# Performance work log

Measured on AMD Instinct MI355X. Metric: run time of the kernel, lower is better.

Reference implementation:

```python
import jax, jax.numpy as jnp
import numpy as np

N_EMBD = 1024
N_HEAD = 16
HEAD_SIZE = N_EMBD // N_HEAD  # 64
HEAD_INDEX = 0
# ALiBi slope: x = (2**8)**(1/n_head); slope = 1 / x**(head_index+1)
SLOPE = 1.0 / ((2.0 ** 8) ** (1.0 / N_HEAD)) ** (HEAD_INDEX + 1)
B, T = 4, 4096


def setup_inputs() -> dict:
    key = jax.random.key(0)
    kx, kq, kk, kv = jax.random.split(key, 4)
    x = jax.random.normal(kx, (B, T, N_EMBD), dtype=jnp.float32)
    wq = jax.random.normal(kq, (HEAD_SIZE, N_EMBD), dtype=jnp.float32) * 0.02
    wk = jax.random.normal(kk, (HEAD_SIZE, N_EMBD), dtype=jnp.float32) * 0.02
    wv = jax.random.normal(kv, (HEAD_SIZE, N_EMBD), dtype=jnp.float32) * 0.02
    return {"x": x, "wq": wq, "wk": wk, "wv": wv}


def reference(x, wq, wk, wv):
    Bq, Tq, C = x.shape
    q = jnp.einsum('btc,hc->bth', x, wq)  # [B,T,Hd]
    k = jnp.einsum('btc,hc->bth', x, wk)
    v = jnp.einsum('btc,hc->bth', x, wv)
    # NOTE: original scales by C**-0.5 where C = n_embd (full dim), not head_size
    wei = jnp.einsum('bth,bsh->bts', q, k) * (C ** -0.5)  # [B,T,T]
    idx = jnp.arange(Tq)
    distance = idx[None, :] - idx[:, None]  # [T,T], j - i
    wei = wei + distance.astype(wei.dtype) * jnp.asarray(SLOPE, wei.dtype)
    causal = distance <= 0  # tril: key index j <= query index i
    wei = jnp.where(causal[None, :, :], wei, -jnp.inf)
    wei = jax.nn.softmax(wei, axis=-1)
    out = jnp.einsum('bts,bsh->bth', wei, v)  # [B,T,Hd]
    return out
```

## Files before the change

### kernel.cpp

```cpp
#include <hip/hip_runtime.h>
#include <hip/hip_bf16.h>
#include <stdint.h>
#include <math.h>

typedef __attribute__((ext_vector_type(8))) short bf16x8;
typedef __attribute__((ext_vector_type(4))) float f32x4;

#define TSEQ 4096
#define LOG2E 1.44269504088896340736f
#define SLOPE 0.70710678118654752440f
#define SL2E (SLOPE * LOG2E)

__device__ __forceinline__ unsigned short f32_to_bf16(float f) {
  union { float f; unsigned int u; } v; v.f = f;
  unsigned int r = v.u + 0x7fffu + ((v.u >> 16) & 1u);
  return (unsigned short)(r >> 16);
}

__device__ __forceinline__ unsigned int pk2(float a, float b) {
  union { __hip_bfloat162 h; unsigned int u; } c;
  c.h = __float22bfloat162_rn(make_float2(a, b));
  return c.u;
}
__device__ __forceinline__ bf16x8 cvt8(f32x4 a, f32x4 b) {
  union { unsigned int u[4]; bf16x8 v; } r;
  r.u[0] = pk2(a[0], a[1]); r.u[1] = pk2(a[2], a[3]);
  r.u[2] = pk2(b[0], b[1]); r.u[3] = pk2(b[2], b[3]);
  return r.v;
}

__device__ __forceinline__ void async_cp16(const void* g, void* l) {
  __builtin_amdgcn_global_load_lds(
      (const __attribute__((address_space(1))) unsigned int*)g,
      (__attribute__((address_space(3))) unsigned int*)l, 16, 0, 0);
}

__global__ __launch_bounds__(256) void init_kernel(
    const float* __restrict__ wq, const float* __restrict__ wk,
    const float* __restrict__ wv, unsigned short* __restrict__ Wb,
    unsigned short* __restrict__ vt) {
  int tid = blockIdx.x * 256 + threadIdx.x;
  if (tid < 24576) {
    int lane = tid & 63, s = (tid >> 6) & 31, nt = (tid >> 11) & 3, t = tid >> 13;
    int n = nt * 16 + (lane & 15);
    int k = s * 32 + (lane >> 4) * 8;
    const float* src = (t == 0 ? wq : (t == 1 ? wk : wv)) + (size_t)n * 1024 + k;
    f32x4 a = *(const f32x4*)src;
    f32x4 b = *(const f32x4*)(src + 4);
    if (t == 0) {
#pragma unroll
      for (int j = 0; j < 4; ++j) { a[j] *= 0.03125f; b[j] *= 0.03125f; }
    }
    *(bf16x8*)(Wb + (size_t)tid * 8) = cvt8(a, b);
  }
  int b2 = tid >> 15, off = (tid & 32767) * 2;
  *(unsigned int*)(vt + (size_t)b2 * 327680 + 262144 + off) = 0x3F803F80u;
}

__global__ __launch_bounds__(256, 2) void proj_kernel(
    const float* __restrict__ x, const unsigned short* __restrict__ Wb,
    unsigned short* __restrict__ qb, unsigned short* __restrict__ kb,
    unsigned short* __restrict__ vt) {
  __shared__ float xbuf[2][64][64];
  __shared__ unsigned short wbuf[2][12][2][64][8];

  const int lane = threadIdx.x & 63;
  const int wave = threadIdx.x >> 6;
  const int l16 = lane & 15, quad = lane >> 4;
  const int R0 = blockIdx.x * 64;

  f32x4 acc[12];
#pragma unroll
  for (int i = 0; i < 12; ++i) acc[i] = (f32x4){0.f, 0.f, 0.f, 0.f};

  const float* xsrc[4];
#pragma unroll
  for (int i = 0; i < 4; ++i) {
    int row = wave * 16 + i * 4 + quad;
    int g = l16 ^ (row & 15);
    xsrc[i] = x + (size_t)(R0 + row) * 1024 + g * 4;
  }
  const unsigned short* wsrc[6];
#pragma unroll
  for (int j = 0; j < 6; ++j) {
    int q = wave * 6 + j;
    wsrc[j] = Wb + ((size_t)((q >> 1) * 32 + (q & 1)) * 64 + lane) * 8;
  }

#pragma unroll
  for (int i = 0; i < 4; ++i)
    async_cp16(xsrc[i], &xbuf[0][wave * 16 + i * 4][0]);
#pragma unroll
  for (int j = 0; j < 6; ++j) {
    int q = wave * 6 + j;
    async_cp16(wsrc[j], &wbuf[0][q >> 1][q & 1][0][0]);
  }
  __syncthreads();

#pragma unroll 1
  for (int step = 0; step < 16; ++step) {
    const int cur = step & 1;
    if (step + 1 < 16) {
      const int nxt = 1 - cur;
#pragma unroll
      for (int i = 0; i < 4; ++i)
        async_cp16(xsrc[i] + (step + 1) * 64, &xbuf[nxt][wave * 16 + i * 4][0]);
#pragma unroll
      for (int j = 0; j < 6; ++j) {
        int q = wave * 6 + j;
        async_cp16(wsrc[j] + (size_t)(step + 1) * 2 * 64 * 8,
                   &wbuf[nxt][q >> 1][q & 1][0][0]);
      }
    }
#pragma unroll
    for (int ss = 0; ss < 2; ++ss) {
      const float* base = &xbuf[cur][wave * 16 + l16][0];
      f32x4 a0 = *(const f32x4*)(base + ((ss * 8 + quad * 2) ^ l16) * 4);
      f32x4 a1 = *(const f32x4*)(base + ((ss * 8 + quad * 2 + 1) ^ l16) * 4);
      bf16x8 af = cvt8(a0, a1);
#pragma unroll
      for (int ci = 0; ci < 12; ++ci) {
        bf16x8 wfr = *(const bf16x8*)&wbuf[cur][ci][ss][lane][0];
        acc[ci] = __builtin_amdgcn_mfma_f32_16x16x32_bf16(af, wfr, acc[ci], 0, 0, 0);
      }
    }
    __syncthreads();
  }

#pragma unroll
  for (int ci = 0; ci < 12; ++ci) {
#pragma unroll
    for (int r = 0; r < 4; ++r) {
      int row = R0 + wave * 16 + quad * 4 + r;
      unsigned short hv = f32_to_bf16(acc[ci][r]);
      if (ci < 4) {
        qb[(size_t)row * 64 + ci * 16 + l16] = hv;
      } else if (ci < 8) {
        kb[(size_t)row * 64 + (ci - 4) * 16 + l16] = hv;
      } else {
        int b = row >> 12, tt = row & 4095;
        vt[((size_t)b * 80 + (ci - 8) * 16 + l16) * TSEQ + tt] = hv;
      }
    }
  }
}

__global__ __launch_bounds__(256, 4) void attn_kernel(
    const unsigned short* __restrict__ qb, const unsigned short* __restrict__ kb,
    const unsigned short* __restrict__ vt, float* __restrict__ out) {
  __shared__ unsigned short pbuf[4][16][40];
  __shared__ float obuf[4][5][16][17];

  const int lane = threadIdx.x & 63;
  const int wave = threadIdx.x >> 6;
  const int l16 = lane & 15, quad = lane >> 4;
  const int tid = blockIdx.x;
  const int b = tid & 3;
  const int r0 = (tid >> 2) << 4;
  const int j0 = (r0 > 112) ? (r0 - 112) : 0;
  const int jb = j0 + wave * 32;

  const unsigned short* kbase = kb + (size_t)b * TSEQ * 64;
  const unsigned short* vbase = vt + (size_t)b * 80 * TSEQ;

  const unsigned short* qrow = qb + (size_t)(b * TSEQ + r0 + l16) * 64 + quad * 8;
  bf16x8 qa0 = *(const bf16x8*)qrow;
  bf16x8 qa1 = *(const bf16x8*)(qrow + 32);

  f32x4 o[5];
#pragma unroll
  for (int dt = 0; dt < 5; ++dt) o[dt] = (f32x4){0.f, 0.f, 0.f, 0.f};

  const int irel = jb + l16 - r0 - quad * 4;
  const float fb = SL2E * (float)irel;

#pragma unroll
  for (int nt = 0; nt < 2; ++nt) {
    const unsigned short* krow = kbase + (size_t)(jb + nt * 16 + l16) * 64 + quad * 8;
    f32x4 sa = (f32x4){0.f, 0.f, 0.f, 0.f};
    sa = __builtin_amdgcn_mfma_f32_16x16x32_bf16(qa0, *(const bf16x8*)krow, sa, 0, 0, 0);
    sa = __builtin_amdgcn_mfma_f32_16x16x32_bf16(qa1, *(const bf16x8*)(krow + 32), sa, 0, 0, 0);
#pragma unroll
    for (int r = 0; r < 4; ++r) {
      float arg = fmaf(sa[r], LOG2E, fb + SL2E * (float)(nt * 16 - r));
      float p = exp2f(arg);
      if (irel + nt * 16 - r > 0) p = 0.f;
      pbuf[wave][quad * 4 + r][nt * 16 + l16] = f32_to_bf16(p);
    }
  }
  bf16x8 pa = *(const bf16x8*)&pbuf[wave][l16][quad * 8];

#pragma unroll
  for (int dt = 0; dt < 5; ++dt) {
    const unsigned short* vrow = vbase + (size_t)(dt * 16 + l16) * TSEQ + jb + quad * 8;
    o[dt] = __builtin_amdgcn_mfma_f32_16x16x32_bf16(pa, *(const bf16x8*)vrow, o[dt], 0, 0, 0);
  }

#pragma unroll
  for (int dt = 0; dt < 5; ++dt)
#pragma unroll
    for (int r = 0; r < 4; ++r)
      obuf[wave][dt][quad * 4 + r][l16] = o[dt][r];

  __syncthreads();

  const int rr = threadIdx.x >> 4;
  const int c0 = (threadIdx.x & 15) * 4;
  const int dt = c0 >> 4, cc = c0 & 15;
  float l = obuf[0][4][rr][0] + obuf[1][4][rr][0] + obuf[2][4][rr][0] + obuf[3][4][rr][0];
  float invl = 1.0f / l;
  f32x4 res;
#pragma unroll
  for (int i = 0; i < 4; ++i)
    res[i] = (obuf[0][dt][rr][cc + i] + obuf[1][dt][rr][cc + i] +
              obuf[2][dt][rr][cc + i] + obuf[3][dt][rr][cc + i]) * invl;
  *(f32x4*)(out + (size_t)(b * TSEQ + r0 + rr) * 64 + c0) = res;
}

extern "C" void kernel_launch(void* const* d_in, const int* in_sizes, int n_in,
                              void* d_out, int out_size, void* d_ws, size_t ws_size,
                              hipStream_t stream) {
  const float* x  = (const float*)d_in[0];
  const float* wq = (const float*)d_in[1];
  const float* wk = (const float*)d_in[2];
  const float* wv = (const float*)d_in[3];
  float* out = (float*)d_out;

  char* ws = (char*)d_ws;
  unsigned short* Wb = (unsigned short*)(ws);
  unsigned short* qb = (unsigned short*)(ws + 393216);
  unsigned short* kb = (unsigned short*)(ws + 393216 + 2097152);
  unsigned short* vt = (unsigned short*)(ws + 393216 + 2 * 2097152);

  init_kernel<<<512, 256, 0, stream>>>(wq, wk, wv, Wb, vt);
  proj_kernel<<<256, 256, 0, stream>>>(x, Wb, qb, kb, vt);
  attn_kernel<<<1024, 256, 0, stream>>>(qb, kb, vt, out);
}
```

Baseline: 125.3 us.

## Triple-buffer projection loads with explicit vmcnt waits; synthesize ones row in registers

The projection kernel moves from double to triple buffering. Loads are issued two steps ahead, and the full __syncthreads is replaced by manual s_waitcnt vmcnt counts plus raw s_barrier, so global loads can stay in flight across iterations. The ones row in vt, used to compute the softmax denominator, is no longer written by init_kernel. The attention kernel instead builds it as a register constant, which shrinks the init launch and cuts the vt stride from 80 to 64 rows. The larger LDS footprint may lower occupancy, and the hand-counted vmcnt values must exactly match the number of outstanding loads.

```diff
diff --git a/kernel.cpp b/kernel.cpp
--- a/kernel.cpp
+++ b/kernel.cpp
@@ -37,32 +37,28 @@
 
 __global__ __launch_bounds__(256) void init_kernel(
     const float* __restrict__ wq, const float* __restrict__ wk,
-    const float* __restrict__ wv, unsigned short* __restrict__ Wb,
-    unsigned short* __restrict__ vt) {
+    const float* __restrict__ wv, unsigned short* __restrict__ Wb) {
   int tid = blockIdx.x * 256 + threadIdx.x;
-  if (tid < 24576) {
-    int lane = tid & 63, s = (tid >> 6) & 31, nt = (tid >> 11) & 3, t = tid >> 13;
-    int n = nt * 16 + (lane & 15);
-    int k = s * 32 + (lane >> 4) * 8;
-    const float* src = (t == 0 ? wq : (t == 1 ? wk : wv)) + (size_t)n * 1024 + k;
-    f32x4 a = *(const f32x4*)src;
-    f32x4 b = *(const f32x4*)(src + 4);
-    if (t == 0) {
-#pragma unroll
-      for (int j = 0; j < 4; ++j) { a[j] *= 0.03125f; b[j] *= 0.03125f; }
-    }
-    *(bf16x8*)(Wb + (size_t)tid * 8) = cvt8(a, b);
-  }
-  int b2 = tid >> 15, off = (tid & 32767) * 2;
-  *(unsigned int*)(vt + (size_t)b2 * 327680 + 262144 + off) = 0x3F803F80u;
-}
-
-__global__ __launch_bounds__(256, 2) void proj_kernel(
+  if (tid >= 24576) return;
+  int lane = tid & 63, s = (tid >> 6) & 31, nt = (tid >> 11) & 3, t = tid >> 13;
+  int n = nt * 16 + (lane & 15);
+  int k = s * 32 + (lane >> 4) * 8;
+  const float* src = (t == 0 ? wq : (t == 1 ? wk : wv)) + (size_t)n * 1024 + k;
+  f32x4 a = *(const f32x4*)src;
+  f32x4 b = *(const f32x4*)(src + 4);
+  if (t == 0) {
+#pragma unroll
+    for (int j = 0; j < 4; ++j) { a[j] *= 0.03125f; b[j] *= 0.03125f; }
+  }
+  *(bf16x8*)(Wb + (size_t)tid * 8) = cvt8(a, b);
+}
+
+__global__ __launch_bounds__(256) void proj_kernel(
     const float* __restrict__ x, const unsigned short* __restrict__ Wb,
     unsigned short* __restrict__ qb, unsigned short* __restrict__ kb,
     unsigned short* __restrict__ vt) {
-  __shared__ float xbuf[2][64][64];
-  __shared__ unsigned short wbuf[2][12][2][64][8];
+  __shared__ float xbuf[3][64][64];
+  __shared__ unsigned short wbuf[3][12][2][64][8];
 
   const int lane = threadIdx.x & 63;
   const int wave = threadIdx.x >> 6;
@@ -87,31 +83,31 @@
     wsrc[j] = Wb + ((size_t)((q >> 1) * 32 + (q & 1)) * 64 + lane) * 8;
   }
 
-#pragma unroll
-  for (int i = 0; i < 4; ++i)
-    async_cp16(xsrc[i], &xbuf[0][wave * 16 + i * 4][0]);
-#pragma unroll
-  for (int j = 0; j < 6; ++j) {
-    int q = wave * 6 + j;
-    async_cp16(wsrc[j], &wbuf[0][q >> 1][q & 1][0][0]);
-  }
-  __syncthreads();
+  auto stage = [&](int s, int bi) {
+#pragma unroll
+    for (int i = 0; i < 4; ++i)
+      async_cp16(xsrc[i] + s * 64, &xbuf[bi][wave * 16 + i * 4][0]);
+#pragma unroll
+    for (int j = 0; j < 6; ++j) {
+      int q = wave * 6 + j;
+      async_cp16(wsrc[j] + (size_t)s * 1024, &wbuf[bi][q >> 1][q & 1][0][0]);
+    }
+  };
+
+  stage(0, 0);
+  stage(1, 1);
 
 #pragma unroll 1
   for (int step = 0; step < 16; ++step) {
-    const int cur = step & 1;
-    if (step + 1 < 16) {
-      const int nxt = 1 - cur;
-#pragma unroll
-      for (int i = 0; i < 4; ++i)
-        async_cp16(xsrc[i] + (step + 1) * 64, &xbuf[nxt][wave * 16 + i * 4][0]);
-#pragma unroll
-      for (int j = 0; j < 6; ++j) {
-        int q = wave * 6 + j;
-        async_cp16(wsrc[j] + (size_t)(step + 1) * 2 * 64 * 8,
-                   &wbuf[nxt][q >> 1][q & 1][0][0]);
-      }
-    }
+    const int cur = step % 3;
+    if (step + 2 < 16) stage(step + 2, (step + 2) % 3);
+    __builtin_amdgcn_sched_barrier(0);
+    if (step < 14)       asm volatile("s_waitcnt vmcnt(20)" ::: "memory");
+    else if (step == 14) asm volatile("s_waitcnt vmcnt(10)" ::: "memory");
+    else                 asm volatile("s_waitcnt vmcnt(0)" ::: "memory");
+    __builtin_amdgcn_sched_barrier(0);
+    __builtin_amdgcn_s_barrier();
+    __builtin_amdgcn_sched_barrier(0);
 #pragma unroll
     for (int ss = 0; ss < 2; ++ss) {
       const float* base = &xbuf[cur][wave * 16 + l16][0];
@@ -124,7 +120,8 @@
         acc[ci] = __builtin_amdgcn_mfma_f32_16x16x32_bf16(af, wfr, acc[ci], 0, 0, 0);
       }
     }
-    __syncthreads();
+    __builtin_amdgcn_sched_barrier(0);
+    __builtin_amdgcn_s_barrier();
   }
 
 #pragma unroll
@@ -139,7 +136,7 @@
         kb[(size_t)row * 64 + (ci - 4) * 16 + l16] = hv;
       } else {
         int b = row >> 12, tt = row & 4095;
-        vt[((size_t)b * 80 + (ci - 8) * 16 + l16) * TSEQ + tt] = hv;
+        vt[((size_t)b * 64 + (ci - 8) * 16 + l16) * TSEQ + tt] = hv;
       }
     }
   }
@@ -161,7 +158,7 @@
   const int jb = j0 + wave * 32;
 
   const unsigned short* kbase = kb + (size_t)b * TSEQ * 64;
-  const unsigned short* vbase = vt + (size_t)b * 80 * TSEQ;
+  const unsigned short* vbase = vt + (size_t)b * 64 * TSEQ;
 
   const unsigned short* qrow = qb + (size_t)(b * TSEQ + r0 + l16) * 64 + quad * 8;
   bf16x8 qa0 = *(const bf16x8*)qrow;
@@ -191,9 +188,14 @@
   bf16x8 pa = *(const bf16x8*)&pbuf[wave][l16][quad * 8];
 
 #pragma unroll
-  for (int dt = 0; dt < 5; ++dt) {
+  for (int dt = 0; dt < 4; ++dt) {
     const unsigned short* vrow = vbase + (size_t)(dt * 16 + l16) * TSEQ + jb + quad * 8;
     o[dt] = __builtin_amdgcn_mfma_f32_16x16x32_bf16(pa, *(const bf16x8*)vrow, o[dt], 0, 0, 0);
+  }
+  {
+    union { unsigned int u[4]; bf16x8 v; } ones;
+    ones.u[0] = ones.u[1] = ones.u[2] = ones.u[3] = 0x3F803F80u;
+    o[4] = __builtin_amdgcn_mfma_f32_16x16x32_bf16(pa, ones.v, o[4], 0, 0, 0);
   }
 
 #pragma unroll
@@ -232,7 +234,7 @@
   unsigned short* kb = (unsigned short*)(ws + 393216 + 2097152);
   unsigned short* vt = (unsigned short*)(ws + 393216 + 2 * 2097152);
 
-  init_kernel<<<512, 256, 0, stream>>>(wq, wk, wv, Wb, vt);
+  init_kernel<<<96, 256, 0, stream>>>(wq, wk, wv, Wb);
   proj_kernel<<<256, 256, 0, stream>>>(x, Wb, qb, kb, vt);
   attn_kernel<<<1024, 256, 0, stream>>>(qb, kb, vt, out);
 }
```

Result: no change. 125.1 us (-0.1%).
